# Optimization experiments

Measured on AMD Instinct MI355X. Metric: run time of the kernel, lower is better.

The kernel has to match this reference:

```python
import jax, jax.numpy as jnp
import numpy as np

INPUT_DIM = 512
HIDDEN_DIM = 256
REP_DIM = 256
SCORE_HIDDEN = 128


def setup_inputs() -> dict:
    key = jax.random.key(0)
    ks = jax.random.split(key, 12)
    def rn(k, shape, scale=None):
        s = scale if scale is not None else 1.0 / np.sqrt(shape[0])
        return jax.random.normal(k, shape, dtype=jnp.float32) * s
    return {
        "feat_x": jax.random.normal(ks[0], (512, INPUT_DIM), dtype=jnp.float32),
        "feat_pos": jax.random.normal(ks[1], (512, INPUT_DIM), dtype=jnp.float32),
        "feat_neg": jax.random.normal(ks[2], (512, INPUT_DIM), dtype=jnp.float32),
        # g: Linear(input,hidden) -> GELU -> Linear(hidden,rep); stored as x @ W
        "g_w1": rn(ks[3], (INPUT_DIM, HIDDEN_DIM)),
        "g_b1": jnp.zeros((HIDDEN_DIM,), jnp.float32),
        "g_w2": rn(ks[4], (HIDDEN_DIM, REP_DIM)),
        "g_b2": jnp.zeros((REP_DIM,), jnp.float32),
        # out_proj: Linear(rep, input, bias=False)
        "out_w": rn(ks[5], (REP_DIM, INPUT_DIM)),
        # score_net: Linear(3*rep+1, score_hidden) -> GELU -> Linear(score_hidden, 1)
        "s_w1": rn(ks[6], (3 * REP_DIM + 1, SCORE_HIDDEN)),
        "s_b1": jnp.zeros((SCORE_HIDDEN,), jnp.float32),
        "s_w2": rn(ks[7], (SCORE_HIDDEN, 1)),
        "s_b2": jnp.zeros((1,), jnp.float32),
    }


def _gelu(x):
    return jax.nn.gelu(x, approximate=False)  # torch nn.GELU default = exact erf


def _g(x, g_w1, g_b1, g_w2, g_b2):
    return _gelu(x @ g_w1 + g_b1) @ g_w2 + g_b2


def _set_operator(feat_x, feat_set, params):
    g_w1, g_b1, g_w2, g_b2, out_w, s_w1, s_b1, s_w2, s_b2 = params
    x_rep = _g(feat_x, g_w1, g_b1, g_w2, g_b2)   # (n, r)
    y_rep = _g(feat_set, g_w1, g_b1, g_w2, g_b2)  # (m, r)
    n, r = x_rep.shape
    m = y_rep.shape[0]
    x_exp = jnp.broadcast_to(x_rep[:, None, :], (n, m, r))
    y_exp = jnp.broadcast_to(y_rep[None, :, :], (n, m, r))
    delta = y_exp - x_exp                                   # (n, m, r)
    delta_norm = jnp.linalg.norm(delta, axis=-1, keepdims=True)
    score_in = jnp.concatenate([x_exp, y_exp, delta, delta_norm], axis=-1)  # (n, m, 3r+1)
    logits = (_gelu(score_in @ s_w1 + s_b1) @ s_w2 + s_b2)[..., 0]          # (n, m)
    weights = jax.nn.softmax(logits, axis=1)
    set_update_rep = jnp.einsum("nm,nmr->nr", weights, delta)
    return set_update_rep @ out_w


def reference(feat_x, feat_pos, feat_neg, g_w1, g_b1, g_w2, g_b2, out_w, s_w1, s_b1, s_w2, s_b2):
    params = (g_w1, g_b1, g_w2, g_b2, out_w, s_w1, s_b1, s_w2, s_b2)
    s_pos = _set_operator(feat_x, feat_pos, params)
    s_neg = _set_operator(feat_x, feat_neg, params)  # mask_self_neg=False
    return s_pos - s_neg
```

## Files before the change

kernel.cpp:

```cpp
#include <hip/hip_runtime.h>
#include <math.h>

#define NN 512
#define IN 512
#define HD 256
#define RD 256
#define SH 128

__device__ __forceinline__ float gelu_fast(float x){
    const float z  = x * 0.70710678118654752f;
    const float az = fabsf(z);
    const float t  = __builtin_amdgcn_rcpf(fmaf(0.3275911f, az, 1.0f));
    float p = fmaf(1.061405429f, t, -1.453152027f);
    p = fmaf(p, t, 1.421413741f);
    p = fmaf(p, t, -0.284496736f);
    p = fmaf(p, t, 0.254829592f);
    p = p * t;
    const float e = __builtin_amdgcn_exp2f(z * z * -1.4426950408889634f);
    const float E = p * e;
    const float one_plus_erf = (x >= 0.0f) ? (2.0f - E) : E;
    return 0.5f * x * one_plus_erf;
}

__device__ __forceinline__ float gelu2b(float u){
    const float au = fabsf(u);
    const float tt = __builtin_amdgcn_rcpf(fmaf(0.3326725f, au, 1.0f));
    const float P  = fmaf(fmaf(0.7478556f, tt, -0.0958798f), tt, 0.3480242f) * tt;
    const float e2 = __builtin_amdgcn_exp2f(u * u * -0.72134752044448170f);
    return fmaf(-au, P * e2, u + au);
}

__global__ __launch_bounds__(512) void k_rep(
    const float* __restrict__ fx, const float* __restrict__ fp, const float* __restrict__ fn,
    const float* __restrict__ w1, const float* __restrict__ b1,
    const float* __restrict__ w2, const float* __restrict__ b2,
    const float* __restrict__ s_w1,
    float* __restrict__ r_x, float* __restrict__ r_p, float* __restrict__ r_n,
    float* __restrict__ rT_p, float* __restrict__ rT_n,
    float* __restrict__ A_x, float* __restrict__ BT_p, float* __restrict__ BT_n,
    float* __restrict__ nx2, float* __restrict__ np2, float* __restrict__ nn2)
{
    __shared__ float xs[4][IN];
    __shared__ float ps[8][4][HD];
    __shared__ float hs[4][HD];
    __shared__ float rloc[4][RD];
    __shared__ float ab4[4][SH];
    const int t = threadIdx.x;
    const int mat = blockIdx.x >> 7;
    const int row0 = (blockIdx.x & 127) << 2;
    const float* src = (mat==0) ? fx : (mat==1) ? fp : fn;

    {
        const int j = t >> 7, c4 = (t & 127) << 2;
        *(float4*)&xs[j][c4] = *(const float4*)&src[(row0+j)*IN + c4];
    }
    __syncthreads();

    const int cg = t & 63, s = t >> 6;
    const int c0 = cg << 2;

    {
        float4 acc[4];
        #pragma unroll
        for (int j=0;j<4;j++) acc[j] = make_float4(0.f,0.f,0.f,0.f);
        const float* wp = w1 + (s*64)*HD + c0;
        #pragma unroll 8
        for (int ii=0; ii<64; ii++){
            float4 w = *(const float4*)wp; wp += HD;
            const int i = s*64 + ii;
            #pragma unroll
            for (int j=0;j<4;j++){
                const float xv = xs[j][i];
                acc[j].x = fmaf(xv, w.x, acc[j].x);
                acc[j].y = fmaf(xv, w.y, acc[j].y);
                acc[j].z = fmaf(xv, w.z, acc[j].z);
                acc[j].w = fmaf(xv, w.w, acc[j].w);
            }
        }
        #pragma unroll
        for (int j=0;j<4;j++) *(float4*)&ps[s][j][c0] = acc[j];
    }
    __syncthreads();

    #pragma unroll
    for (int rep=0; rep<2; rep++){
        const int idx = rep*512 + t;
        const int j = idx >> 8, c = idx & 255;
        float v = b1[c];
        #pragma unroll
        for (int ss=0; ss<8; ss++) v += ps[ss][j][c];
        hs[j][c] = gelu_fast(v);
    }
    __syncthreads();

    {
        float4 acc[4];
        #pragma unroll
        for (int j=0;j<4;j++) acc[j] = make_float4(0.f,0.f,0.f,0.f);
        const float* wp = w2 + (s*32)*RD + c0;
        #pragma unroll 8
        for (int ii=0; ii<32; ii++){
            float4 w = *(const float4*)wp; wp += RD;
            const int i = s*32 + ii;
            #pragma unroll
            for (int j=0;j<4;j++){
                const float xv = hs[j][i];
                acc[j].x = fmaf(xv, w.x, acc[j].x);
                acc[j].y = fmaf(xv, w.y, acc[j].y);
                acc[j].z = fmaf(xv, w.z, acc[j].z);
                acc[j].w = fmaf(xv, w.w, acc[j].w);
            }
        }
        #pragma unroll
        for (int j=0;j<4;j++) *(float4*)&ps[s][j][c0] = acc[j];
    }
    __syncthreads();

    float* rout = (mat==0) ? r_x : (mat==1) ? r_p : r_n;
    #pragma unroll
    for (int rep=0; rep<2; rep++){
        const int idx = rep*512 + t;
        const int j = idx >> 8, c = idx & 255;
        float v = b2[c];
        #pragma unroll
        for (int ss=0; ss<8; ss++) v += ps[ss][j][c];
        rloc[j][c] = v;
        rout[(row0+j)*RD + c] = v;
    }
    __syncthreads();

    if (t < 256){
        const int w = t >> 6, l = t & 63;
        float v = 0.f;
        #pragma unroll
        for (int q=0;q<4;q++){ const float e = rloc[w][l + 64*q]; v = fmaf(e,e,v); }
        #pragma unroll
        for (int off=32; off>=1; off>>=1) v += __shfl_xor(v, off);
        if (l==0){
            float* nrm = (mat==0) ? nx2 : (mat==1) ? np2 : nn2;
            nrm[row0 + w] = v;
        }
    }
    if (mat && t < 256){
        float* rT = (mat==1) ? rT_p : rT_n;
        float4 q = make_float4(rloc[0][t], rloc[1][t], rloc[2][t], rloc[3][t]);
        *(float4*)&rT[t*NN + row0] = q;
    }

    {
        const int cg2 = t & 31, s2 = t >> 5;
        const int cc0 = cg2 << 2;
        const float sgn = (mat==0) ? -1.0f : 1.0f;
        const int base1 = (mat==0) ? 0 : 256;
        const float* p1 = s_w1 + (base1 + s2*16)*SH + cc0;
        const float* p3 = s_w1 + (512   + s2*16)*SH + cc0;
        float4 a[4];
        #pragma unroll
        for (int j=0;j<4;j++) a[j] = make_float4(0.f,0.f,0.f,0.f);
        #pragma unroll 8
        for (int ii=0; ii<16; ii++){
            float4 wa = *(const float4*)p1; p1 += SH;
            float4 wd = *(const float4*)p3; p3 += SH;
            float4 w;
            w.x = fmaf(sgn, wd.x, wa.x);
            w.y = fmaf(sgn, wd.y, wa.y);
            w.z = fmaf(sgn, wd.z, wa.z);
            w.w = fmaf(sgn, wd.w, wa.w);
            const int i = s2*16 + ii;
            #pragma unroll
            for (int j=0;j<4;j++){
                const float xv = rloc[j][i];
                a[j].x = fmaf(xv, w.x, a[j].x);
                a[j].y = fmaf(xv, w.y, a[j].y);
                a[j].z = fmaf(xv, w.z, a[j].z);
                a[j].w = fmaf(xv, w.w, a[j].w);
            }
        }
        float* psf = &ps[0][0][0];
        #pragma unroll
        for (int j=0;j<4;j++) *(float4*)&psf[(s2*4 + j)*SH + cc0] = a[j];
    }
    __syncthreads();

    {
        const float* psf = &ps[0][0][0];
        const int j = t >> 7, c = t & 127;
        float v = 0.f;
        #pragma unroll
        for (int ss=0; ss<16; ss++) v += psf[(ss*4 + j)*SH + c];
        if (mat==0) A_x[(row0+j)*SH + c] = v;
        else        ab4[j][c] = v;
    }
    __syncthreads();
    if (mat && t < 128){
        float* BT = (mat==1) ? BT_p : BT_n;
        float4 q = make_float4(ab4[0][t], ab4[1][t], ab4[2][t], ab4[3][t]);
        *(float4*)&BT[t*NN + row0] = q;
    }
}

__global__ __launch_bounds__(256) void k_sd(
    const float* __restrict__ r_x, const float* __restrict__ rT_p, const float* __restrict__ rT_n,
    const float* __restrict__ A_x, const float* __restrict__ BT_p, const float* __restrict__ BT_n,
    const float* __restrict__ r_p, const float* __restrict__ r_n,
    const float* __restrict__ nx2, const float* __restrict__ np2, const float* __restrict__ nn2,
    const float* __restrict__ s_w1, const float* __restrict__ s_b1,
    const float* __restrict__ s_w2,
    float* __restrict__ psum, float* __restrict__ Spart)
{
    __shared__ float4 xs4[RD];
    __shared__ float4 cmb4[4][SH];
    __shared__ float  pd[4][4][64];
    __shared__ float  ny2v[64];
    __shared__ float4 evb4[64];
    const int t = threadIdx.x;
    const int set = blockIdx.x >> 10;
    const int rem = blockIdx.x & 1023;
    const int n0 = (rem >> 3) << 2;
    const int mt = rem & 7;
    const int mbase = mt << 6;
    const int tm = t & 63, kh = t >> 6;
    const int m = mbase + tm;
    const float* yT = set ? rT_n : rT_p;
    const float* BT = set ? BT_n : BT_p;

    const float nxv = nx2[n0 + kh];

    xs4[t] = make_float4(r_x[n0*RD + t],       r_x[(n0+1)*RD + t],
                         r_x[(n0+2)*RD + t],   r_x[(n0+3)*RD + t]);
    if (t < SH){
        const float b1v = s_b1[t];
        const float wn  = s_w1[768*SH + t];
        const float w2h = 0.5f * s_w2[t];
        cmb4[0][t] = make_float4(A_x[ n0     *SH + t] + b1v, wn, w2h, 0.f);
        cmb4[1][t] = make_float4(A_x[(n0+1)*SH + t] + b1v, wn, w2h, 0.f);
        cmb4[2][t] = make_float4(A_x[(n0+2)*SH + t] + b1v, wn, w2h, 0.f);
        cmb4[3][t] = make_float4(A_x[(n0+3)*SH + t] + b1v, wn, w2h, 0.f);
    }
    if (t < 64) ny2v[t] = (set ? nn2 : np2)[mbase + t];
    __syncthreads();

    {
        float d0=0.f, d1=0.f, d2=0.f, d3=0.f;
        const float* yp = yT + (kh << 6)*NN + m;
        #pragma unroll 8
        for (int rr=0; rr<64; rr++){
            const float y = yp[rr*NN];
            const float4 xv = xs4[(kh << 6) + rr];
            d0 = fmaf(xv.x, y, d0);
            d1 = fmaf(xv.y, y, d1);
            d2 = fmaf(xv.z, y, d2);
            d3 = fmaf(xv.w, y, d3);
        }
        pd[0][kh][tm] = d0; pd[1][kh][tm] = d1;
        pd[2][kh][tm] = d2; pd[3][kh][tm] = d3;
    }
    __syncthreads();

    const float dsum = pd[kh][0][tm] + pd[kh][1][tm] + pd[kh][2][tm] + pd[kh][3][tm];
    const float dn = sqrtf(fmaxf(fmaf(-2.f, dsum, nxv + ny2v[tm]), 0.f));

    float acc = 0.f;
    {
        const float* bp = BT + m;
        const float4* cp = cmb4[kh];
        #pragma unroll 4
        for (int k=0; k<SH; k++){
            const float  B  = bp[k*NN];
            const float4 cw = cp[k];
            const float  u  = fmaf(dn, cw.y, cw.x + B);
            acc = fmaf(cw.z, gelu2b(u), acc);
        }
    }

    {
        const float L2E = 1.4426950408889634f;
        const float ev = __builtin_amdgcn_exp2f(acc * L2E);
        ((float*)evb4)[tm*4 + kh] = ev;
        float v = ev;
        #pragma unroll
        for (int off=32; off>=1; off>>=1) v += __shfl_xor(v, off);
        if (tm == 0) Spart[(set*8 + mt)*NN + n0 + kh] = v;
    }
    __syncthreads();

    {
        const float* ry = (set ? r_n : r_p) + mbase*RD + t;
        float e0 = 0.f, e1 = 0.f, e2 = 0.f, e3 = 0.f;
        #pragma unroll 8
        for (int mm=0; mm<64; mm++){
            const float rv = ry[mm*RD];
            const float4 w = evb4[mm];
            e0 = fmaf(w.x, rv, e0);
            e1 = fmaf(w.y, rv, e1);
            e2 = fmaf(w.z, rv, e2);
            e3 = fmaf(w.w, rv, e3);
        }
        float* P = psum + ((set*8 + mt)*NN + n0)*RD;
        P[t]        = e0;
        P[RD + t]   = e1;
        P[2*RD + t] = e2;
        P[3*RD + t] = e3;
    }
}

__global__ __launch_bounds__(256) void k_fin(
    const float* __restrict__ psum, const float* __restrict__ Spart,
    const float* __restrict__ out_w, float* __restrict__ out)
{
    __shared__ float dv[2][RD];
    const int t = threadIdx.x;
    const int np = blockIdx.x >> 2, ct = blockIdx.x & 3;
    const int n0 = np << 1;
    const int cb = ct << 7;

    #pragma unroll
    for (int rep=0; rep<2; rep++){
        const int idx = rep*256 + t;
        const int j = idx >> 8, c = idx & 255;
        const int n = n0 + j;
        float Sp = 0.f, Sn = 0.f;
        #pragma unroll
        for (int q=0;q<8;q++){
            Sp += Spart[q*NN + n];
            Sn += Spart[(8+q)*NN + n];
        }
        float vp = 0.f, vn = 0.f;
        #pragma unroll
        for (int q=0;q<8;q++){
            vp += psum[(q*NN + n)*RD + c];
            vn += psum[((8+q)*NN + n)*RD + c];
        }
        dv[j][c] = vp * (1.0f/Sp) - vn * (1.0f/Sn);
    }
    __syncthreads();

    {
        const int j = t >> 7, cc = t & 127;
        const int col = cb + cc;
        float o = 0.f;
        const float* wo = out_w + col;
        #pragma unroll 8
        for (int r=0; r<RD; r++){ o = fmaf(dv[j][r], *wo, o); wo += IN; }
        out[(n0+j)*IN + col] = o;
    }
}

extern "C" void kernel_launch(void* const* d_in, const int* in_sizes, int n_in,
                              void* d_out, int out_size, void* d_ws, size_t ws_size,
                              hipStream_t stream)
{
    const float* fx  = (const float*)d_in[0];
    const float* fp  = (const float*)d_in[1];
    const float* fn  = (const float*)d_in[2];
    const float* gw1 = (const float*)d_in[3];
    const float* gb1 = (const float*)d_in[4];
    const float* gw2 = (const float*)d_in[5];
    const float* gb2 = (const float*)d_in[6];
    const float* ow  = (const float*)d_in[7];
    const float* sw1 = (const float*)d_in[8];
    const float* sb1 = (const float*)d_in[9];
    const float* sw2 = (const float*)d_in[10];
    float* out = (float*)d_out;

    float* ws   = (float*)d_ws;
    float* r_x  = ws;
    float* r_p  = r_x  + 131072;
    float* r_n  = r_p  + 131072;
    float* rT_p = r_n  + 131072;
    float* rT_n = rT_p + 131072;
    float* A_x  = rT_n + 131072;
    float* BT_p = A_x  + 65536;
    float* BT_n = BT_p + 65536;
    float* Spar = BT_n + 65536;
    float* nx2  = Spar + 8192;
    float* np2  = nx2  + 512;
    float* nn2  = np2  + 512;
    float* psum = nn2  + 512;

    hipLaunchKernelGGL(k_rep, dim3(384), dim3(512), 0, stream,
                       fx, fp, fn, gw1, gb1, gw2, gb2, sw1,
                       r_x, r_p, r_n, rT_p, rT_n, A_x, BT_p, BT_n,
                       nx2, np2, nn2);
    hipLaunchKernelGGL(k_sd, dim3(2048), dim3(256), 0, stream,
                       r_x, rT_p, rT_n, A_x, BT_p, BT_n, r_p, r_n,
                       nx2, np2, nn2, sw1, sb1, sw2, psum, Spar);
    hipLaunchKernelGGL(k_fin, dim3(1024), dim3(256), 0, stream,
                       psum, Spar, ow, out);
}
```

Measured before the change: 155.7 us.

## Split GELU linear term out of score MLP and repartition hidden units across waves

GELU(u) is rewritten as 0.5*(u+|u|) minus an erf-tail term, and the linear 0.5*u part of the second-layer dot product is computed analytically. That part is precomputed as per-row contributions (pA from A_x, pB from B in k_rep, plus a norm coefficient c0). The hidden-unit loop in k_sd is also repartitioned so each wave handles 32 hidden units for all 4 rows, loading each B value once instead of four times. Partial sums are then reduced through shared memory. This removes redundant global loads and the per-element linear adds, at the cost of an extra reduction, two more syncs and more live registers.

```diff
diff --git a/kernel.cpp b/kernel.cpp
--- a/kernel.cpp
+++ b/kernel.cpp
@@ -22,23 +22,16 @@
     return 0.5f * x * one_plus_erf;
 }
 
-__device__ __forceinline__ float gelu2b(float u){
-    const float au = fabsf(u);
-    const float tt = __builtin_amdgcn_rcpf(fmaf(0.3326725f, au, 1.0f));
-    const float P  = fmaf(fmaf(0.7478556f, tt, -0.0958798f), tt, 0.3480242f) * tt;
-    const float e2 = __builtin_amdgcn_exp2f(u * u * -0.72134752044448170f);
-    return fmaf(-au, P * e2, u + au);
-}
-
 __global__ __launch_bounds__(512) void k_rep(
     const float* __restrict__ fx, const float* __restrict__ fp, const float* __restrict__ fn,
     const float* __restrict__ w1, const float* __restrict__ b1,
     const float* __restrict__ w2, const float* __restrict__ b2,
-    const float* __restrict__ s_w1,
+    const float* __restrict__ s_w1, const float* __restrict__ s_w2,
     float* __restrict__ r_x, float* __restrict__ r_p, float* __restrict__ r_n,
     float* __restrict__ rT_p, float* __restrict__ rT_n,
     float* __restrict__ A_x, float* __restrict__ BT_p, float* __restrict__ BT_n,
-    float* __restrict__ nx2, float* __restrict__ np2, float* __restrict__ nn2)
+    float* __restrict__ nx2, float* __restrict__ np2, float* __restrict__ nn2,
+    float* __restrict__ pB_p, float* __restrict__ pB_n)
 {
     __shared__ float xs[4][IN];
     __shared__ float ps[8][4][HD];
@@ -197,6 +190,18 @@
         float4 q = make_float4(ab4[0][t], ab4[1][t], ab4[2][t], ab4[3][t]);
         *(float4*)&BT[t*NN + row0] = q;
     }
+    if (mat && t < 256){
+        const int w = t >> 6, l = t & 63;
+        const float w2a = 0.5f * s_w2[l];
+        const float w2b = 0.5f * s_w2[l + 64];
+        float v = ab4[w][l]*w2a + ab4[w][l+64]*w2b;
+        #pragma unroll
+        for (int off=32; off>=1; off>>=1) v += __shfl_xor(v, off);
+        if (l == 0){
+            float* pB = (mat==1) ? pB_p : pB_n;
+            pB[row0 + w] = v;
+        }
+    }
 }
 
 __global__ __launch_bounds__(256) void k_sd(
@@ -204,12 +209,14 @@
     const float* __restrict__ A_x, const float* __restrict__ BT_p, const float* __restrict__ BT_n,
     const float* __restrict__ r_p, const float* __restrict__ r_n,
     const float* __restrict__ nx2, const float* __restrict__ np2, const float* __restrict__ nn2,
+    const float* __restrict__ pB_p, const float* __restrict__ pB_n,
     const float* __restrict__ s_w1, const float* __restrict__ s_b1,
     const float* __restrict__ s_w2,
     float* __restrict__ psum, float* __restrict__ Spart)
 {
     __shared__ float4 xs4[RD];
-    __shared__ float4 cmb4[4][SH];
+    __shared__ float4 cmbA[SH];
+    __shared__ float2 cmbW[SH];
     __shared__ float  pd[4][4][64];
     __shared__ float  ny2v[64];
     __shared__ float4 evb4[64];
@@ -224,21 +231,38 @@
     const float* yT = set ? rT_n : rT_p;
     const float* BT = set ? BT_n : BT_p;
 
-    const float nxv = nx2[n0 + kh];
+    const float nxa = nx2[n0];
+    const float nxb = nx2[n0 + 1];
+    const float nxc = nx2[n0 + 2];
+    const float nxd = nx2[n0 + 3];
+    const float pBm = (set ? pB_n : pB_p)[m];
 
     xs4[t] = make_float4(r_x[n0*RD + t],       r_x[(n0+1)*RD + t],
                          r_x[(n0+2)*RD + t],   r_x[(n0+3)*RD + t]);
     if (t < SH){
         const float b1v = s_b1[t];
-        const float wn  = s_w1[768*SH + t];
-        const float w2h = 0.5f * s_w2[t];
-        cmb4[0][t] = make_float4(A_x[ n0     *SH + t] + b1v, wn, w2h, 0.f);
-        cmb4[1][t] = make_float4(A_x[(n0+1)*SH + t] + b1v, wn, w2h, 0.f);
-        cmb4[2][t] = make_float4(A_x[(n0+2)*SH + t] + b1v, wn, w2h, 0.f);
-        cmb4[3][t] = make_float4(A_x[(n0+3)*SH + t] + b1v, wn, w2h, 0.f);
+        cmbA[t] = make_float4(A_x[n0*SH + t] + b1v,     A_x[(n0+1)*SH + t] + b1v,
+                              A_x[(n0+2)*SH + t] + b1v, A_x[(n0+3)*SH + t] + b1v);
+        cmbW[t] = make_float2(s_w1[768*SH + t], 0.5f * s_w2[t]);
     }
     if (t < 64) ny2v[t] = (set ? nn2 : np2)[mbase + t];
     __syncthreads();
+
+    float pAk, c0;
+    {
+        const float4 ca = cmbA[tm], cb = cmbA[tm + 64];
+        const float2 wa = cmbW[tm], wb = cmbW[tm + 64];
+        const float va = (kh==0)?ca.x:(kh==1)?ca.y:(kh==2)?ca.z:ca.w;
+        const float vb = (kh==0)?cb.x:(kh==1)?cb.y:(kh==2)?cb.z:cb.w;
+        float pa = va*wa.y + vb*wb.y;
+        float cc = wa.x*wa.y + wb.x*wb.y;
+        #pragma unroll
+        for (int off=32; off>=1; off>>=1){
+            pa += __shfl_xor(pa, off);
+            cc += __shfl_xor(cc, off);
+        }
+        pAk = pa; c0 = cc;
+    }
 
     {
         float d0=0.f, d1=0.f, d2=0.f, d3=0.f;
@@ -256,26 +280,72 @@
         pd[2][kh][tm] = d2; pd[3][kh][tm] = d3;
     }
     __syncthreads();
-
-    const float dsum = pd[kh][0][tm] + pd[kh][1][tm] + pd[kh][2][tm] + pd[kh][3][tm];
-    const float dn = sqrtf(fmaxf(fmaf(-2.f, dsum, nxv + ny2v[tm]), 0.f));
-
-    float acc = 0.f;
-    {
-        const float* bp = BT + m;
-        const float4* cp = cmb4[kh];
+    float dn0, dn1, dn2, dn3;
+    {
+        const float s0 = pd[0][0][tm] + pd[0][1][tm] + pd[0][2][tm] + pd[0][3][tm];
+        const float s1 = pd[1][0][tm] + pd[1][1][tm] + pd[1][2][tm] + pd[1][3][tm];
+        const float s2 = pd[2][0][tm] + pd[2][1][tm] + pd[2][2][tm] + pd[2][3][tm];
+        const float s3 = pd[3][0][tm] + pd[3][1][tm] + pd[3][2][tm] + pd[3][3][tm];
+        const float nyc = ny2v[tm];
+        dn0 = sqrtf(fmaxf(fmaf(-2.f, s0, nxa + nyc), 0.f));
+        dn1 = sqrtf(fmaxf(fmaf(-2.f, s1, nxb + nyc), 0.f));
+        dn2 = sqrtf(fmaxf(fmaf(-2.f, s2, nxc + nyc), 0.f));
+        dn3 = sqrtf(fmaxf(fmaf(-2.f, s3, nxd + nyc), 0.f));
+    }
+
+    float a0=0.f, a1=0.f, a2=0.f, a3=0.f;
+    {
+        const float* bp = BT + (kh << 5)*NN + m;
         #pragma unroll 4
-        for (int k=0; k<SH; k++){
-            const float  B  = bp[k*NN];
-            const float4 cw = cp[k];
-            const float  u  = fmaf(dn, cw.y, cw.x + B);
-            acc = fmaf(cw.z, gelu2b(u), acc);
-        }
-    }
+        for (int kk=0; kk<32; kk++){
+            const float  B  = bp[kk*NN];
+            const float4 cA = cmbA[(kh << 5) + kk];
+            const float2 w  = cmbW[(kh << 5) + kk];
+            {
+                const float u  = fmaf(dn0, w.x, cA.x + B);
+                const float au = fabsf(u);
+                const float tt = __builtin_amdgcn_rcpf(fmaf(0.3326725f, au, 1.0f));
+                const float P  = fmaf(fmaf(0.7478556f, tt, -0.0958798f), tt, 0.3480242f) * tt;
+                const float e2 = __builtin_amdgcn_exp2f(u * u * -0.72134752044448170f);
+                a0 = fmaf(w.y, fmaf(-au, P * e2, au), a0);
+            }
+            {
+                const float u  = fmaf(dn1, w.x, cA.y + B);
+                const float au = fabsf(u);
+                const float tt = __builtin_amdgcn_rcpf(fmaf(0.3326725f, au, 1.0f));
+                const float P  = fmaf(fmaf(0.7478556f, tt, -0.0958798f), tt, 0.3480242f) * tt;
+                const float e2 = __builtin_amdgcn_exp2f(u * u * -0.72134752044448170f);
+                a1 = fmaf(w.y, fmaf(-au, P * e2, au), a1);
+            }
+            {
+                const float u  = fmaf(dn2, w.x, cA.z + B);
+                const float au = fabsf(u);
+                const float tt = __builtin_amdgcn_rcpf(fmaf(0.3326725f, au, 1.0f));
+                const float P  = fmaf(fmaf(0.7478556f, tt, -0.0958798f), tt, 0.3480242f) * tt;
+                const float e2 = __builtin_amdgcn_exp2f(u * u * -0.72134752044448170f);
+                a2 = fmaf(w.y, fmaf(-au, P * e2, au), a2);
+            }
+            {
+                const float u  = fmaf(dn3, w.x, cA.w + B);
+                const float au = fabsf(u);
+                const float tt = __builtin_amdgcn_rcpf(fmaf(0.3326725f, au, 1.0f));
+                const float P  = fmaf(fmaf(0.7478556f, tt, -0.0958798f), tt, 0.3480242f) * tt;
+                const float e2 = __builtin_amdgcn_exp2f(u * u * -0.72134752044448170f);
+                a3 = fmaf(w.y, fmaf(-au, P * e2, au), a3);
+            }
+        }
+    }
+    __syncthreads();
+    pd[0][kh][tm] = a0; pd[1][kh][tm] = a1;
+    pd[2][kh][tm] = a2; pd[3][kh][tm] = a3;
+    __syncthreads();
 
     {
         const float L2E = 1.4426950408889634f;
-        const float ev = __builtin_amdgcn_exp2f(acc * L2E);
+        const float nl  = pd[kh][0][tm] + pd[kh][1][tm] + pd[kh][2][tm] + pd[kh][3][tm];
+        const float dnk = (kh==0)?dn0:(kh==1)?dn1:(kh==2)?dn2:dn3;
+        const float logit = pAk + pBm + dnk*c0 + nl;
+        const float ev = __builtin_amdgcn_exp2f(logit * L2E);
         ((float*)evb4)[tm*4 + kh] = ev;
         float v = ev;
         #pragma unroll
@@ -376,15 +446,17 @@
     float* nx2  = Spar + 8192;
     float* np2  = nx2  + 512;
     float* nn2  = np2  + 512;
-    float* psum = nn2  + 512;
+    float* pB_p = nn2  + 512;
+    float* pB_n = pB_p + 512;
+    float* psum = pB_n + 512;
 
     hipLaunchKernelGGL(k_rep, dim3(384), dim3(512), 0, stream,
-                       fx, fp, fn, gw1, gb1, gw2, gb2, sw1,
+                       fx, fp, fn, gw1, gb1, gw2, gb2, sw1, sw2,
                        r_x, r_p, r_n, rT_p, rT_n, A_x, BT_p, BT_n,
-                       nx2, np2, nn2);
+                       nx2, np2, nn2, pB_p, pB_n);
     hipLaunchKernelGGL(k_sd, dim3(2048), dim3(256), 0, stream,
                        r_x, rT_p, rT_n, A_x, BT_p, BT_n, r_p, r_n,
-                       nx2, np2, nn2, sw1, sb1, sw2, psum, Spar);
+                       nx2, np2, nn2, pB_p, pB_n, sw1, sb1, sw2, psum, Spar);
     hipLaunchKernelGGL(k_fin, dim3(1024), dim3(256), 0, stream,
                        psum, Spar, ow, out);
 }
```

After: 155.6 us. No clear change (-0.1%).
